# Kernel tuning notes

Hardware: AMD Instinct MI355X
Metric: run time of the kernel (lower is better)

The kernel has to match this reference:

```python
import jax, jax.numpy as jnp
import numpy as np

B = 2048
ENB = 16      # enb_cnt (beams)
RBG = 32      # rbg_cnt
MAXREQ = 50   # max_req
OBS_F = 400   # Requests features = 50*8
H = 1024
OUT = ENB * RBG * (MAXREQ + 1)  # 26112
IN = OBS_F + ENB * RBG + ENB * MAXREQ  # 1712


def _linear_init(key, fan_in, fan_out):
    kw, kb = jax.random.split(key)
    lim = 1.0 / np.sqrt(fan_in)
    W = jax.random.uniform(kw, (fan_in, fan_out), jnp.float32, -lim, lim)
    b = jax.random.uniform(kb, (fan_out,), jnp.float32, -lim, lim)
    return W, b


def setup_inputs() -> dict:
    key = jax.random.key(0)
    ks = jax.random.split(key, 6)
    obs = jax.random.normal(ks[0], (B, OBS_F), jnp.float32)
    rbgMap = jax.random.randint(ks[1], (B, ENB, RBG), 0, 2).astype(jnp.float32)
    invFlag = (jax.random.randint(ks[2], (B, ENB, MAXREQ), 0, 3) - 1).astype(jnp.float32)
    W1, b1 = _linear_init(ks[3], IN, H)
    W2, b2 = _linear_init(ks[4], H, H)
    W3, b3 = _linear_init(ks[5], H, OUT)
    return {"obs": obs, "rbgMap": rbgMap, "invFlag": invFlag,
            "W1": W1, "b1": b1, "W2": W2, "b2": b2, "W3": W3, "b3": b3}


def reference(obs, rbgMap, invFlag, W1, b1, W2, b2, W3, b3):
    Bt = obs.shape[0]
    rbg_flat = rbgMap.reshape(Bt, ENB * RBG)                      # [B, E*R]
    inv = invFlag.reshape(Bt, ENB, MAXREQ)
    # am1: invFlag broadcast per-rbg -> [B, E*R, MAXREQ]
    am1 = jnp.broadcast_to(inv[:, :, None, :], (Bt, ENB, RBG, MAXREQ)).reshape(Bt, ENB * RBG, MAXREQ)
    rbg_exp = rbg_flat[:, :, None]                                 # [B, E*R, 1]
    # vectorized form of the nested loops:
    #   where am1 == -1: -> 1 if rbg==0, 0 if rbg==1; else unchanged
    am1 = jnp.where(am1 == -1.0, jnp.where(rbg_exp == 0.0, 1.0, 0.0), am1)
    # prepend never-masked no-op action column, mask = nonzero
    amask = jnp.concatenate([jnp.zeros((Bt, ENB * RBG, 1), am1.dtype), am1], axis=2) != 0
    # dense MLP on concatenated observation
    inp = jnp.concatenate([obs, rbg_flat, invFlag.reshape(Bt, -1)], axis=1)  # [B, 1712]
    h = jnp.tanh(inp @ W1 + b1)
    h = jnp.tanh(h @ W2 + b2)
    logits = (h @ W3 + b3).reshape(Bt, ENB * RBG, MAXREQ + 1)
    logits = jnp.where(amask, -jnp.inf, logits)
    return logits
```

## Files before the change

kernel.cpp:

```cpp
#include <hip/hip_runtime.h>
#include <math.h>

#define B_    2048
#define OBSF_ 400
#define H_    1024
#define IN_   1712
#define INP_  1728
#define KS1_  54
#define KSH_  32
#define OUT_  26112
#define NCOL_ 51
#define MAXQ_ 50

#define NEG_BIG (-3.0e38f)

typedef __attribute__((ext_vector_type(4))) float  floatx4;
typedef __bf16 bf16x8 __attribute__((ext_vector_type(8)));

__device__ __forceinline__ unsigned short f2b(float v) {
    unsigned u = __float_as_uint(v);
    u += 0x7FFFu + ((u >> 16) & 1u);
    return (unsigned short)(u >> 16);
}


__global__ void pack_frag(const float* __restrict__ obs,
                          const float* __restrict__ rbg,
                          const float* __restrict__ inv,
                          unsigned short* __restrict__ P) {
    const int ks = blockIdx.x, r16 = blockIdx.y, lane = threadIdx.x;
    const int r = r16 * 16 + (lane & 15);
    const int kb = ks * 32 + (lane >> 4) * 8;
    __attribute__((aligned(16))) unsigned short tmp[8];
    #pragma unroll
    for (int j = 0; j < 8; j++) {
        int k = kb + j;
        float v = 0.0f;
        if (k < OBSF_)            v = obs[r * OBSF_ + k];
        else if (k < OBSF_ + 512) v = rbg[r * 512 + (k - OBSF_)];
        else if (k < IN_)         v = inv[r * 800 + (k - OBSF_ - 512)];
        tmp[j] = f2b(v);
    }
    *(uint4*)(P + ((size_t)(r16 * KS1_ + ks) * 64 + lane) * 8) = *(const uint4*)tmp;
}

__global__ __launch_bounds__(256)
void transpose_frag(const float* __restrict__ W, unsigned short* __restrict__ P,
                    int K, int N, int KS) {
    __shared__ float tile[32][33];
    const int n0 = blockIdx.x * 32, k0 = blockIdx.y * 32;
    const int tx = threadIdx.x, ty = threadIdx.y;
    #pragma unroll
    for (int i = 0; i < 4; i++) {
        int k = k0 + ty + i * 8;
        float v = 0.0f;
        if (k < K) v = W[(size_t)k * N + n0 + tx];
        tile[ty + i * 8][tx] = v;
    }
    __syncthreads();
    const int tid = ty * 32 + tx;
    if (tid < 128) {
        const int b = tid >> 6, lane = tid & 63;
        const int i16 = lane & 15, q = lane >> 4;
        __attribute__((aligned(16))) unsigned short tmp[8];
        #pragma unroll
        for (int j = 0; j < 8; j++) tmp[j] = f2b(tile[q * 8 + j][b * 16 + i16]);
        *(uint4*)(P + ((size_t)(((n0 >> 4) + b) * KS + (k0 >> 5)) * 64 + lane) * 8) =
            *(const uint4*)tmp;
    }
}

template<int MT, int NT, int KS, int EPI>
__global__ __launch_bounds__(256, 2)
void gemm_frag(const unsigned short* __restrict__ Ap,
               const unsigned short* __restrict__ Bp,
               const float* __restrict__ bias,
               void* __restrict__ outv,
               const float* __restrict__ rbg,
               const float* __restrict__ inv,
               int KSo) {
    const int tid = threadIdx.x;
    const int wave = tid >> 6, lane = tid & 63;
    const int wtm = blockIdx.y * 2 + (wave >> 1);
    const int wtn = blockIdx.x * 2 + (wave & 1);
    const int m16base = wtm * MT, n16base = wtn * NT;

    const unsigned short* pa = Ap + (size_t)m16base * KS * 512 + lane * 8;
    const unsigned short* pb = Bp + (size_t)n16base * KS * 512 + lane * 8;

    floatx4 acc[MT][NT];
    #pragma unroll
    for (int i = 0; i < MT; i++)
        #pragma unroll
        for (int j = 0; j < NT; j++) acc[i][j] = (floatx4){0.f, 0.f, 0.f, 0.f};

    bf16x8 a0[MT], b0[NT], a1[MT], b1[NT];
    #define LOADA(dst, ks_)                                                    \
        _Pragma("unroll") for (int mt = 0; mt < MT; mt++)                      \
            dst[mt] = *(const bf16x8*)(pa + (size_t)mt * KS * 512 + (ks_) * 512);
    #define LOADB(dst, ks_)                                                    \
        _Pragma("unroll") for (int nt = 0; nt < NT; nt++)                      \
            dst[nt] = *(const bf16x8*)(pb + (size_t)nt * KS * 512 + (ks_) * 512);
    #define MFMA(aa, bb)                                                       \
        _Pragma("unroll") for (int mt = 0; mt < MT; mt++)                      \
            _Pragma("unroll") for (int nt = 0; nt < NT; nt++)                  \
                acc[mt][nt] = __builtin_amdgcn_mfma_f32_16x16x32_bf16(         \
                    aa[mt], bb[nt], acc[mt][nt], 0, 0, 0);

    LOADA(a0, 0); LOADB(b0, 0);
    for (int ks = 0; ks < KS; ks += 2) {
        LOADA(a1, ks + 1); LOADB(b1, ks + 1);
        MFMA(a0, b0);
        int k2 = (ks + 2 < KS) ? ks + 2 : 0;
        LOADA(a0, k2); LOADB(b0, k2);
        MFMA(a1, b1);
    }
    #undef LOADA
    #undef LOADB
    #undef MFMA

    const int quad = lane >> 4;
    #pragma unroll
    for (int nt = 0; nt < NT; nt++) {
        const int col = (n16base + nt) * 16 + (lane & 15);
        const float bv = bias[col];
        unsigned short* Hp = (unsigned short*)outv;
        const int ko = col >> 5, kb = (col >> 3) & 3, kj = col & 7;
        #pragma unroll
        for (int mt = 0; mt < MT; mt++) {
            const int m16 = m16base + mt;
            #pragma unroll
            for (int r = 0; r < 4; r++) {
                const int mlo = quad * 4 + r;
                Hp[((size_t)(m16 * KSo + ko) * 64 + (mlo | (kb << 4))) * 8 + kj] =
                    f2b(tanhf(acc[mt][nt][r] + bv));
            }
        }
    }
}

typedef __attribute__((address_space(1))) const unsigned int gu32;
typedef __attribute__((address_space(3))) unsigned int su32;
__device__ __forceinline__ void async_copy16(unsigned short* l, const unsigned short* g) {
    __builtin_amdgcn_global_load_lds((gu32*)g, (su32*)l, 16, 0, 0);
}

template<int MT, int NT, int KS>
__global__ __launch_bounds__(256, 2)
void gemm_lds(const unsigned short* __restrict__ Ap,
              const unsigned short* __restrict__ Bp,
              const float* __restrict__ bias,
              float* __restrict__ C,
              const float* __restrict__ rbg,
              const float* __restrict__ inv) {
    constexpr int ACH = 2 * MT;
    constexpr int CH  = ACH + 2 * NT;
    constexpr int CPW = CH / 4;
    static_assert(CH % 4 == 0, "chunk count must split across 4 waves");
    __shared__ __align__(16) unsigned short lds[2][CH][512];

    const int tid  = threadIdx.x;
    const int wave = tid >> 6, lane = tid & 63;

    const int i = blockIdx.x;
    const int xcd = i & 7, j = i >> 3;
    const int m     = xcd * 2 + (j & 1);
    const int panel = j >> 1;
    const int blk_m16 = m * ACH;
    const int blk_n16 = panel * 2 * NT;

    const int rg = wave >> 1, cg = wave & 1;
    const int m16base = blk_m16 + rg * MT;
    const int n16base = blk_n16 + cg * NT;

    const int chunk0 = wave * CPW;
    const unsigned short* gb[CPW];
    #pragma unroll
    for (int q = 0; q < CPW; q++) {
        const int c = chunk0 + q;
        gb[q] = (c < ACH ? Ap + (size_t)(blk_m16 + c) * KS * 512
                         : Bp + (size_t)(blk_n16 + (c - ACH)) * KS * 512)
                + lane * 8;
    }

    floatx4 acc[MT][NT];
    #pragma unroll
    for (int a = 0; a < MT; a++)
        #pragma unroll
        for (int b = 0; b < NT; b++) acc[a][b] = (floatx4){0.f, 0.f, 0.f, 0.f};

    #define STAGE(bufi, ksv) do {                                              \
        _Pragma("unroll")                                                      \
        for (int q = 0; q < CPW; q++)                                          \
            async_copy16(&lds[bufi][chunk0 + q][0], gb[q] + (size_t)(ksv) * 512); \
    } while (0)

    #define COMPUTE(bufi) do {                                                 \
        bf16x8 af[MT], bv[NT];                                                 \
        _Pragma("unroll")                                                      \
        for (int mt = 0; mt < MT; mt++)                                        \
            af[mt] = *(const bf16x8*)&lds[bufi][rg * MT + mt][lane * 8];       \
        _Pragma("unroll")                                                      \
        for (int nt = 0; nt < NT; nt++)                                        \
            bv[nt] = *(const bf16x8*)&lds[bufi][ACH + cg * NT + nt][lane * 8]; \
        _Pragma("unroll")                                                      \
        for (int mt = 0; mt < MT; mt++)                                        \
            _Pragma("unroll")                                                  \
            for (int nt = 0; nt < NT; nt++)                                    \
                acc[mt][nt] = __builtin_amdgcn_mfma_f32_16x16x32_bf16(         \
                    af[mt], bv[nt], acc[mt][nt], 0, 0, 0);                     \
    } while (0)

    STAGE(0, 0);
    __syncthreads();
    #pragma unroll 1
    for (int ks = 0; ks < KS; ks += 2) {
        STAGE(1, ks + 1);
        COMPUTE(0);
        __syncthreads();
        if (ks + 2 < KS) STAGE(0, ks + 2);
        COMPUTE(1);
        __syncthreads();
    }
    #undef STAGE
    #undef COMPUTE

    const int quad = lane >> 4;
    #pragma unroll
    for (int nt = 0; nt < NT; nt++) {
        const int col = (n16base + nt) * 16 + (lane & 15);
        const float bvs = bias[col];
        const int jj = col / NCOL_;
        const int qq = col - jj * NCOL_;
        const int e  = jj >> 5;
        #pragma unroll
        for (int mt = 0; mt < MT; mt++) {
            const int row0 = (m16base + mt) * 16 + quad * 4;
            #pragma unroll
            for (int r = 0; r < 4; r++) {
                const int row = row0 + r;
                float v = acc[mt][nt][r] + bvs;
                if (qq > 0) {
                    float iv = inv[(size_t)row * 800 + e * MAXQ_ + (qq - 1)];
                    if (iv == 1.0f ||
                        (iv == -1.0f && rbg[(size_t)row * 512 + jj] == 0.0f))
                        v = NEG_BIG;
                }
                __builtin_nontemporal_store(v, &C[(size_t)row * OUT_ + col]);
            }
        }
    }
}

extern "C" void kernel_launch(void* const* d_in, const int* in_sizes, int n_in,
                              void* d_out, int out_size, void* d_ws, size_t ws_size,
                              hipStream_t stream) {
    const float* obs = (const float*)d_in[0];
    const float* rbg = (const float*)d_in[1];
    const float* inv = (const float*)d_in[2];
    const float* W1  = (const float*)d_in[3];
    const float* b1  = (const float*)d_in[4];
    const float* W2  = (const float*)d_in[5];
    const float* b2  = (const float*)d_in[6];
    const float* W3  = (const float*)d_in[7];
    const float* b3  = (const float*)d_in[8];
    float* out = (float*)d_out;

    char* ws = (char*)d_ws;
    unsigned short* inpP = (unsigned short*)ws;  ws += (size_t)B_ * INP_ * 2;
    unsigned short* W1P  = (unsigned short*)ws;  ws += (size_t)H_ * INP_ * 2;
    unsigned short* W2P  = (unsigned short*)ws;  ws += (size_t)H_ * H_ * 2;
    unsigned short* W3P  = (unsigned short*)ws;  ws += (size_t)OUT_ * H_ * 2;
    unsigned short* h1P  = (unsigned short*)ws;  ws += (size_t)B_ * H_ * 2;
    unsigned short* h2P  = (unsigned short*)ws;

    pack_frag<<<dim3(KS1_, B_ / 16), 64, 0, stream>>>(obs, rbg, inv, inpP);

    dim3 tb(32, 8);
    transpose_frag<<<dim3(H_ / 32, INP_ / 32), tb, 0, stream>>>(W1, W1P, IN_, H_, KS1_);
    transpose_frag<<<dim3(H_ / 32, H_ / 32),   tb, 0, stream>>>(W2, W2P, H_, H_, KSH_);
    transpose_frag<<<dim3(OUT_ / 32, H_ / 32), tb, 0, stream>>>(W3, W3P, H_, OUT_, KSH_);

    gemm_frag<4, 2, KS1_, 0><<<dim3(H_ / 64, B_ / 128), 256, 0, stream>>>(
        inpP, W1P, b1, h1P, nullptr, nullptr, KSH_);
    gemm_frag<4, 2, KSH_, 0><<<dim3(H_ / 64, B_ / 128), 256, 0, stream>>>(
        h1P, W2P, b2, h2P, nullptr, nullptr, KSH_);
    gemm_lds<4, 4, KSH_><<<dim3(16 * (OUT_ / 128)), 256, 0, stream>>>(
        h2P, W3P, b3, out, rbg, inv);
}
```

Measured before the change: 567.6 us.

## Widen transpose/pack tiles and remap final GEMM block order per XCD

The pack kernel now runs four 64-lane waves per 256-thread block instead of one wave per block. The weight transpose now handles 128-column tiles so that all 256 threads write output fragments, where before only half of them did. The final GEMM changes its block-to-tile mapping so each XCD takes a contiguous range of panels across all 16 M tiles, aiming for better L2 reuse of W3 panels. Together these cut block-launch overhead and idle threads in the preprocessing kernels, but they change the cache access pattern of the large GEMM.

```diff
diff --git a/kernel.cpp b/kernel.cpp
--- a/kernel.cpp
+++ b/kernel.cpp
@@ -24,11 +24,15 @@
 }
 
 
-__global__ void pack_frag(const float* __restrict__ obs,
-                          const float* __restrict__ rbg,
-                          const float* __restrict__ inv,
-                          unsigned short* __restrict__ P) {
-    const int ks = blockIdx.x, r16 = blockIdx.y, lane = threadIdx.x;
+__global__ __launch_bounds__(256)
+void pack_frag(const float* __restrict__ obs,
+               const float* __restrict__ rbg,
+               const float* __restrict__ inv,
+               unsigned short* __restrict__ P) {
+    const int tid = threadIdx.x;
+    const int wave = tid >> 6, lane = tid & 63;
+    const int cid = blockIdx.x * 4 + wave;
+    const int ks = cid % KS1_, r16 = cid / KS1_;
     const int r = r16 * 16 + (lane & 15);
     const int kb = ks * 32 + (lane >> 4) * 8;
     __attribute__((aligned(16))) unsigned short tmp[8];
@@ -47,25 +51,27 @@
 __global__ __launch_bounds__(256)
 void transpose_frag(const float* __restrict__ W, unsigned short* __restrict__ P,
                     int K, int N, int KS) {
-    __shared__ float tile[32][33];
-    const int n0 = blockIdx.x * 32, k0 = blockIdx.y * 32;
-    const int tx = threadIdx.x, ty = threadIdx.y;
-    #pragma unroll
-    for (int i = 0; i < 4; i++) {
-        int k = k0 + ty + i * 8;
+    __shared__ float tile[32][129];
+    const int n0 = blockIdx.x * 128, k0 = blockIdx.y * 32;
+    const int tid = threadIdx.x;
+    const int nn = tid & 127, kk0 = tid >> 7;
+    #pragma unroll
+    for (int i = 0; i < 16; i++) {
+        int k = k0 + kk0 + i * 2;
         float v = 0.0f;
-        if (k < K) v = W[(size_t)k * N + n0 + tx];
-        tile[ty + i * 8][tx] = v;
+        if (k < K) v = W[(size_t)k * N + n0 + nn];
+        tile[kk0 + i * 2][nn] = v;
     }
     __syncthreads();
-    const int tid = ty * 32 + tx;
-    if (tid < 128) {
-        const int b = tid >> 6, lane = tid & 63;
-        const int i16 = lane & 15, q = lane >> 4;
+    const int wave = tid >> 6, lane = tid & 63;
+    const int i16 = lane & 15, q = lane >> 4;
+    #pragma unroll
+    for (int c2 = 0; c2 < 2; c2++) {
+        const int c = wave * 2 + c2;
         __attribute__((aligned(16))) unsigned short tmp[8];
         #pragma unroll
-        for (int j = 0; j < 8; j++) tmp[j] = f2b(tile[q * 8 + j][b * 16 + i16]);
-        *(uint4*)(P + ((size_t)(((n0 >> 4) + b) * KS + (k0 >> 5)) * 64 + lane) * 8) =
+        for (int j = 0; j < 8; j++) tmp[j] = f2b(tile[q * 8 + j][c * 16 + i16]);
+        *(uint4*)(P + ((size_t)(((n0 >> 4) + c) * KS + (k0 >> 5)) * 64 + lane) * 8) =
             *(const uint4*)tmp;
     }
 }
@@ -164,8 +170,9 @@
 
     const int i = blockIdx.x;
     const int xcd = i & 7, j = i >> 3;
-    const int m     = xcd * 2 + (j & 1);
-    const int panel = j >> 1;
+    const int g = xcd * 408 + j;
+    const int panel = g >> 4;
+    const int m     = g & 15;
     const int blk_m16 = m * ACH;
     const int blk_n16 = panel * 2 * NT;
 
@@ -274,12 +281,11 @@
     unsigned short* h1P  = (unsigned short*)ws;  ws += (size_t)B_ * H_ * 2;
     unsigned short* h2P  = (unsigned short*)ws;
 
-    pack_frag<<<dim3(KS1_, B_ / 16), 64, 0, stream>>>(obs, rbg, inv, inpP);
-
-    dim3 tb(32, 8);
-    transpose_frag<<<dim3(H_ / 32, INP_ / 32), tb, 0, stream>>>(W1, W1P, IN_, H_, KS1_);
-    transpose_frag<<<dim3(H_ / 32, H_ / 32),   tb, 0, stream>>>(W2, W2P, H_, H_, KSH_);
-    transpose_frag<<<dim3(OUT_ / 32, H_ / 32), tb, 0, stream>>>(W3, W3P, H_, OUT_, KSH_);
+    pack_frag<<<dim3(KS1_ * (B_ / 16) / 4), 256, 0, stream>>>(obs, rbg, inv, inpP);
+
+    transpose_frag<<<dim3(H_ / 128, INP_ / 32), 256, 0, stream>>>(W1, W1P, IN_, H_, KS1_);
+    transpose_frag<<<dim3(H_ / 128, H_ / 32),   256, 0, stream>>>(W2, W2P, H_, H_, KSH_);
+    transpose_frag<<<dim3(OUT_ / 128, H_ / 32), 256, 0, stream>>>(W3, W3P, H_, OUT_, KSH_);
 
     gemm_frag<4, 2, KS1_, 0><<<dim3(H_ / 64, B_ / 128), 256, 0, stream>>>(
         inpP, W1P, b1, h1P, nullptr, nullptr, KSH_);
```

Result: slower. 592.8 us (+4.4%).
